# Performance work log

Hardware: AMD Instinct MI355X
Metric: run time of the kernel (lower is better)

Reference implementation:

```python
import jax, jax.numpy as jnp
import numpy as np

H = 16      # num_heads
HD = 128    # head_dim = embed_dim // num_heads
BS = 64     # NSA block_size
SEL = 8     # selected blocks per query (block_counts)
WIN = 64    # sliding window (left) size
BASE = 10000.0


def _rope(t):
    # t: [b, n, h, hd]; rotary LRPE (lrpe_type=1)
    n, hd = t.shape[1], t.shape[-1]
    half = hd // 2
    inv = 1.0 / (BASE ** (jnp.arange(half, dtype=jnp.float32) / half))
    th = jnp.arange(n, dtype=jnp.float32)[:, None] * inv[None, :]  # [n, half]
    cos = jnp.cos(th)[None, :, None, :]
    sin = jnp.sin(th)[None, :, None, :]
    t1, t2 = t[..., :half], t[..., half:]
    return jnp.concatenate([t1 * cos - t2 * sin, t1 * sin + t2 * cos], axis=-1)


def _nsa_forward(x, Wq, Wk, Wv, Wg, Wo):
    b, n, d = x.shape
    nb = n // BS
    scale = HD ** -0.5
    q = (x @ Wq).reshape(b, n, H, HD)
    k = (x @ Wk).reshape(b, n, H, HD)
    v = (x @ Wv).reshape(b, n, H, HD)
    g = jax.nn.sigmoid(x @ Wg)                   # [b, n, 3H]
    g_cmp, g_slc, g_swa = jnp.split(g, 3, axis=-1)
    q = _rope(q)
    k = _rope(k)
    idx = jnp.arange(n)

    # --- compression branch: mean-pooled KV blocks, causal over fully-past blocks
    k_cmp = k.reshape(b, nb, BS, H, HD).mean(axis=2)   # [b, nb, h, hd]
    v_cmp = v.reshape(b, nb, BS, H, HD).mean(axis=2)
    s_cmp = jnp.einsum('bnhd,bmhd->bhnm', q, k_cmp) * scale  # [b, h, n, nb]
    blk_end = (jnp.arange(nb) + 1) * BS - 1
    cmp_mask = idx[:, None] >= blk_end[None, :]        # [n, nb]
    p_cmp = jax.nn.softmax(jnp.where(cmp_mask[None, None], s_cmp, -1e30), axis=-1)
    p_cmp = p_cmp * cmp_mask.any(-1)[None, None, :, None]  # zero rows with no valid block
    o_cmp = jnp.einsum('bhnm,bmhd->bnhd', p_cmp, v_cmp)

    # --- selection branch: top-k blocks by compressed scores, current block forced
    cur_blk = jax.nn.one_hot(idx // BS, nb, dtype=jnp.float32)  # [n, nb]
    imp = p_cmp + 2.0 * cur_blk[None, None]
    sel = jax.lax.top_k(imp, SEL)[1]                   # [b, h, n, SEL]
    blk_sel = jax.nn.one_hot(sel, nb).sum(-2) > 0      # [b, h, n, nb]
    causal = idx[:, None] >= idx[None, :]              # [n, n]
    slc_mask = blk_sel[..., idx // BS] & causal[None, None]  # [b, h, n, n]
    s_full = jnp.einsum('bnhd,bmhd->bhnm', q, k) * scale     # [b, h, n, n]
    p_slc = jax.nn.softmax(jnp.where(slc_mask, s_full, -1e30), axis=-1)
    o_slc = jnp.einsum('bhnm,bmhd->bnhd', p_slc, v)

    swa_mask = causal & (idx[:, None] - idx[None, :] <= WIN)
    p_swa = jax.nn.softmax(jnp.where(swa_mask[None, None], s_full, -1e30), axis=-1)
    o_swa = jnp.einsum('bhnm,bmhd->bnhd', p_swa, v)

    o = (o_cmp * g_cmp[..., None] + o_slc * g_slc[..., None]
         + o_swa * g_swa[..., None])                   # [b, n, h, hd]
    return o.reshape(b, n, H * HD) @ Wo


def setup_inputs() -> dict:
    key = jax.random.key(0)
    ks = jax.random.split(key, 6)
    B, N, D = 2, 1024, 2048
    std = 0.02
    return {
        'x': jax.random.normal(ks[0], (B, N, D), jnp.float32),
        'Wq': jax.random.normal(ks[1], (D, H * HD), jnp.float32) * std,
        'Wk': jax.random.normal(ks[2], (D, H * HD), jnp.float32) * std,
        'Wv': jax.random.normal(ks[3], (D, H * HD), jnp.float32) * std,
        'Wg': jax.random.normal(ks[4], (D, 3 * H), jnp.float32) * std,
        'Wo': jax.random.normal(ks[5], (H * HD, D), jnp.float32) * std,
    }


def reference(x, Wq, Wk, Wv, Wg, Wo):
    return _nsa_forward(x, Wq, Wk, Wv, Wg, Wo)
```

## Files before the change

### kernel.cpp

```cpp
#include <hip/hip_runtime.h>
#include <hip/hip_bf16.h>

#define HN   16
#define HDIM 128
#define NSEQ 1024
#define NBLK 16
#define BSZ  64
#define SCALE 0.08838834764831845f
#define QKV_STR 6400
#define KOFS 2048
#define VOFS 4096
#define GOFS 6144

typedef __attribute__((ext_vector_type(8))) short bfrag;
typedef __attribute__((ext_vector_type(4))) float facc;

__device__ __forceinline__ float bf2f(short s) {
  union { unsigned u; float f; } cv;
  cv.u = ((unsigned)(unsigned short)s) << 16;
  return cv.f;
}
__device__ __forceinline__ short f2bf(float f) {
  unsigned u = __float_as_uint(f);
  u = (u + 0x7fff + ((u >> 16) & 1)) >> 16;
  return (short)u;
}

#define ASYNC16(gp, lp)                                                    \
  __builtin_amdgcn_global_load_lds(                                        \
      (const __attribute__((address_space(1))) void*)(gp),                 \
      (__attribute__((address_space(3))) void*)(lp), 16, 0, 0)

#define MFMA16(a, b, c) __builtin_amdgcn_mfma_f32_16x16x32_bf16(a, b, c, 0, 0, 0)

__global__ __launch_bounds__(256) void prep(const float* __restrict__ Wq,
                                            const float* __restrict__ Wk,
                                            const float* __restrict__ Wv,
                                            const float* __restrict__ Wg,
                                            const float* __restrict__ Wo,
                                            const float* __restrict__ x,
                                            short* __restrict__ w_t,
                                            short* __restrict__ wo_t,
                                            short* __restrict__ x_bf,
                                            float2* __restrict__ tbl) {
  __shared__ float tile[32][33];
  const int z = blockIdx.z;
  const int bx = blockIdx.x * 32, by = blockIdx.y * 32;
  const int tx = threadIdx.x & 31, ty = threadIdx.x >> 5;
  if (z == 5) {
    if (blockIdx.y >= 4) return;
    int i = (blockIdx.y * 64 + blockIdx.x) * 256 + threadIdx.x;
    int d = i & 63, n = i >> 6;
    float inv = expf(-(float)d * (9.210340371976184f / 64.0f));
    float sn, cs;
    sincosf((float)n * inv, &sn, &cs);
    tbl[i] = make_float2(cs, sn);
    return;
  }
  if (z == 4) {
#pragma unroll
    for (int i = 0; i < 4; ++i) {
      const int row = by + ty + 8 * i;
      x_bf[(size_t)row * 2048 + bx + tx] = f2bf(x[(size_t)row * 2048 + bx + tx]);
    }
    return;
  }
  if (z == 3) {
    if (blockIdx.x >= 4) return;
#pragma unroll
    for (int i = 0; i < 4; ++i) {
      const int c = bx + tx;
      tile[ty + 8 * i][tx] = (c < 48) ? Wg[(size_t)(by + ty + 8 * i) * 48 + c] : 0.f;
    }
    __syncthreads();
#pragma unroll
    for (int i = 0; i < 4; ++i)
      w_t[(size_t)(GOFS + bx + ty + 8 * i) * 2048 + by + tx] = f2bf(tile[tx][ty + 8 * i]);
    return;
  }
  if (z == 6) {
#pragma unroll
    for (int i = 0; i < 4; ++i)
      tile[ty + 8 * i][tx] = Wo[(size_t)(by + ty + 8 * i) * 2048 + bx + tx];
    __syncthreads();
#pragma unroll
    for (int i = 0; i < 4; ++i)
      wo_t[(size_t)(bx + ty + 8 * i) * 2048 + by + tx] = f2bf(tile[tx][ty + 8 * i]);
    return;
  }
  const float* src = (z == 0) ? Wq : (z == 1) ? Wk : Wv;
#pragma unroll
  for (int i = 0; i < 4; ++i)
    tile[ty + 8 * i][tx] = src[(size_t)(by + ty + 8 * i) * 2048 + bx + tx];
  __syncthreads();
#pragma unroll
  for (int i = 0; i < 4; ++i)
    w_t[(size_t)(z * 2048 + bx + ty + 8 * i) * 2048 + by + tx] = f2bf(tile[tx][ty + 8 * i]);
}

__global__ __launch_bounds__(512, 1) void gemm256(const short* __restrict__ A,
                                                  const short* __restrict__ Bt,
                                                  short* __restrict__ C,
                                                  int M, int N, int K) {
  __shared__ short lds[2][2][16384];
  const int t = threadIdx.x;
  const int l = t & 63, w = t >> 6;
  const int wm = w >> 2, wn = w & 3;
  const int lm = l & 15, hi = l >> 4;
  const int lanexor = (lm & 7) << 3;
  const int kk0 = (hi * 8) ^ lanexor;
  const int L = blockIdx.x;
  const int item = (L & 7) * (gridDim.x >> 3) + (L >> 3);
  const int nrow = M >> 8;
  const int row0 = (item % nrow) * 256, col0 = (item / nrow) * 256;
  const int nt = K >> 6;
  const int ni = nt >> 1;

  const int srow = t >> 3;
  const int scol = 8 * ((t & 7) ^ (srow & 7));
  const short* Ab = A + (size_t)(row0 + srow) * K + scol;
  const short* Bb = Bt + (size_t)(col0 + srow) * K + scol;

#define STAGE(mat, srcbase, h, tau, buf)                                     \
  {                                                                          \
    const short* g_ = (srcbase) + (size_t)(h) * 128 * K + (size_t)(tau) * 64;\
    short* d_ = &lds[buf][mat][(h) * 8192 + t * 8];                          \
    ASYNC16(g_, d_);                                                         \
    ASYNC16(g_ + (size_t)64 * K, d_ + 4096);                                 \
  }

#define DS_A(qm, cb)                                                         \
  _Pragma("unroll") for (int ii = 0; ii < 4; ++ii) {                         \
    const int row_ = wm * 128 + (qm) * 64 + ii * 16 + lm;                    \
    af[ii * 2 + 0] = *(const bfrag*)&lds[cb][0][row_ * 64 + kk0];            \
    af[ii * 2 + 1] = *(const bfrag*)&lds[cb][0][row_ * 64 + (kk0 ^ 32)];     \
  }
#define DS_B(qn, arr, cb)                                                    \
  _Pragma("unroll") for (int jj = 0; jj < 2; ++jj) {                         \
    const int row_ = wn * 64 + (qn) * 32 + jj * 16 + lm;                     \
    arr[jj * 2 + 0] = *(const bfrag*)&lds[cb][1][row_ * 64 + kk0];           \
    arr[jj * 2 + 1] = *(const bfrag*)&lds[cb][1][row_ * 64 + (kk0 ^ 32)];    \
  }
#define QUAD(qm, qn, arr)                                                    \
  _Pragma("unroll") for (int ii = 0; ii < 4; ++ii)                           \
  _Pragma("unroll") for (int jj = 0; jj < 2; ++jj) {                         \
    acc[(qm)*4+ii][(qn)*2+jj] = MFMA16(af[ii*2+0], arr[jj*2+0], acc[(qm)*4+ii][(qn)*2+jj]); \
    acc[(qm)*4+ii][(qn)*2+jj] = MFMA16(af[ii*2+1], arr[jj*2+1], acc[(qm)*4+ii][(qn)*2+jj]); \
  }
#define BARLG                                                                \
  __builtin_amdgcn_s_barrier();                                              \
  asm volatile("s_waitcnt lgkmcnt(0)" ::: "memory");                         \
  __builtin_amdgcn_sched_barrier(0)
#define PRIO1 __builtin_amdgcn_s_setprio(1)
#define PRIO0 __builtin_amdgcn_s_setprio(0)
#define BAR __builtin_amdgcn_s_barrier()

  facc acc[8][4] = {};
  bfrag af[8], bf0[4], bf1[4];

  STAGE(0, Ab, 0, 0, 0); STAGE(0, Ab, 1, 0, 0);
  STAGE(1, Bb, 0, 0, 0); STAGE(1, Bb, 1, 0, 0);
  STAGE(1, Bb, 0, 1, 1); STAGE(1, Bb, 1, 1, 1);
  asm volatile("s_waitcnt vmcnt(4)" ::: "memory");
  BAR;

  for (int i = 0; i < ni; ++i) {
    const int t1 = 2 * i + 1;
    const int g2 = (2 * i + 2 < nt) ? 2 * i + 2 : 2 * i;
    const int g3 = (2 * i + 3 < nt) ? 2 * i + 3 : t1;

    DS_A(0, 0); DS_B(0, bf0, 0);
    STAGE(0, Ab, 0, t1, 1);
    BARLG; PRIO1; QUAD(0, 0, bf0); PRIO0; BAR;

    DS_B(1, bf1, 0);
    STAGE(0, Ab, 1, t1, 1);
    BARLG; PRIO1; QUAD(0, 1, bf1); PRIO0; BAR;

    DS_A(1, 0);
    STAGE(1, Bb, 0, g2, 0);
    BARLG; PRIO1; QUAD(1, 1, bf1); PRIO0; BAR;

    STAGE(1, Bb, 1, g2, 0);
    PRIO1; QUAD(1, 0, bf0); PRIO0;
    asm volatile("s_waitcnt vmcnt(4)" ::: "memory");
    BAR;

    DS_A(0, 1); DS_B(0, bf0, 1);
    STAGE(0, Ab, 0, g2, 0);
    BARLG; PRIO1; QUAD(0, 0, bf0); PRIO0; BAR;

    DS_B(1, bf1, 1);
    STAGE(0, Ab, 1, g2, 0);
    BARLG; PRIO1; QUAD(0, 1, bf1); PRIO0; BAR;

    DS_A(1, 1);
    STAGE(1, Bb, 0, g3, 1);
    BARLG; PRIO1; QUAD(1, 1, bf1); PRIO0; BAR;

    STAGE(1, Bb, 1, g3, 1);
    PRIO1; QUAD(1, 0, bf0); PRIO0;
    asm volatile("s_waitcnt vmcnt(4)" ::: "memory");
    BAR;
  }

#pragma unroll
  for (int i = 0; i < 8; ++i)
#pragma unroll
    for (int j = 0; j < 4; ++j)
#pragma unroll
      for (int rr = 0; rr < 4; ++rr)
        C[(size_t)(row0 + wm * 128 + i * 16 + hi * 4 + rr) * N +
          col0 + wn * 64 + j * 16 + lm] = f2bf(acc[i][j][rr]);
#undef STAGE
#undef DS_A
#undef DS_B
#undef QUAD
#undef BARLG
#undef PRIO1
#undef PRIO0
#undef BAR
}

__device__ __forceinline__ void store_c(float* p, float v) { *p = v; }
__device__ __forceinline__ void store_c(short* p, float v) { *p = f2bf(v); }

template <typename OT>
__global__ __launch_bounds__(512, 1) void gemm_bf16_bt(const short* __restrict__ A,
                                                       const short* __restrict__ Bt,
                                                       OT* __restrict__ C,
                                                       int M, int N, int K) {
  __shared__ short As[128 * 32];
  __shared__ short Bs[128 * 32];
  const int t = threadIdx.x;
  const int l = t & 63, w = t >> 6;
  const int wr = w >> 2, wc = w & 3;
  const int lm = l & 15, lk = (l >> 4) * 8;
  const int nwg = gridDim.x;
  const int L = blockIdx.x;
  const int wg = (L & 7) * (nwg >> 3) + (L >> 3);
  const int nrow = M >> 7;
  const int row0 = (wg % nrow) * 128, col0 = (wg / nrow) * 128;
  facc acc[4][2] = {};

  const int sr = t >> 2;
  const int sk = (t & 3) * 8;
  const short* Ag = A + (size_t)(row0 + sr) * K + sk;
  const short* Bg = Bt + (size_t)(col0 + sr) * K + sk;
  short* la = As + t * 8;
  short* lb = Bs + t * 8;

  for (int k0 = 0; k0 < K; k0 += 32) {
    ASYNC16(Ag + k0, la);
    ASYNC16(Bg + k0, lb);
    __syncthreads();
    bfrag af[4], bf[2];
#pragma unroll
    for (int i = 0; i < 4; ++i)
      af[i] = *(const bfrag*)&As[(wr * 64 + i * 16 + lm) * 32 + lk];
#pragma unroll
    for (int j = 0; j < 2; ++j)
      bf[j] = *(const bfrag*)&Bs[(wc * 32 + j * 16 + lm) * 32 + lk];
#pragma unroll
    for (int i = 0; i < 4; ++i)
#pragma unroll
      for (int j = 0; j < 2; ++j)
        acc[i][j] = MFMA16(af[i], bf[j], acc[i][j]);
    __syncthreads();
  }

  const int orow = row0 + wr * 64 + (l >> 4) * 4;
  const int ocol = col0 + wc * 32 + lm;
#pragma unroll
  for (int i = 0; i < 4; ++i)
#pragma unroll
    for (int j = 0; j < 2; ++j)
#pragma unroll
      for (int rr = 0; rr < 4; ++rr)
        store_c(&C[(size_t)(orow + i * 16 + rr) * N + ocol + j * 16], acc[i][j][rr]);
}

__global__ __launch_bounds__(256) void postqkv(short* __restrict__ qkv,
                                               const float2* __restrict__ tbl,
                                               float* __restrict__ kc,
                                               short* __restrict__ vt,
                                               short* __restrict__ vct) {
  const int nb = blockIdx.x, h = blockIdx.y, b = blockIdx.z;
  const int t = threadIdx.x;
  const int n0 = nb * 64;
  __shared__ short tile[64][136];

  const int row = t >> 2;
  const int c16 = (t & 3) * 16;
  const float2* tp = tbl + (size_t)(n0 + row) * 64 + c16;

#pragma unroll
  for (int qk = 0; qk < 2; ++qk) {
    short* base = qkv + (size_t)(b * NSEQ + n0 + row) * QKV_STR + qk * KOFS + h * HDIM + c16;
    bfrag lo0 = *(const bfrag*)base;
    bfrag lo1 = *(const bfrag*)(base + 8);
    bfrag hi0 = *(const bfrag*)(base + 64);
    bfrag hi1 = *(const bfrag*)(base + 72);
    bfrag olo0, olo1, ohi0, ohi1;
#pragma unroll
    for (int j = 0; j < 8; ++j) {
      float2 cs0 = tp[j], cs1 = tp[j + 8];
      float a0 = bf2f(lo0[j]), b0 = bf2f(hi0[j]);
      float a1 = bf2f(lo1[j]), b1 = bf2f(hi1[j]);
      olo0[j] = f2bf(a0 * cs0.x - b0 * cs0.y);
      ohi0[j] = f2bf(a0 * cs0.y + b0 * cs0.x);
      olo1[j] = f2bf(a1 * cs1.x - b1 * cs1.y);
      ohi1[j] = f2bf(a1 * cs1.y + b1 * cs1.x);
    }
    *(bfrag*)base = olo0;
    *(bfrag*)(base + 8) = olo1;
    *(bfrag*)(base + 64) = ohi0;
    *(bfrag*)(base + 72) = ohi1;
    if (qk == 1) {
      *(bfrag*)&tile[row][c16] = olo0;
      *(bfrag*)&tile[row][c16 + 8] = olo1;
      *(bfrag*)&tile[row][c16 + 64] = ohi0;
      *(bfrag*)&tile[row][c16 + 72] = ohi1;
    }
  }
  __syncthreads();

  if (t < 128) {
    float s = 0.f;
#pragma unroll 8
    for (int r = 0; r < 64; ++r) s += bf2f(tile[r][t]);
    kc[(((size_t)(b * NBLK + nb) * HN) + h) * 128 + t] = s * (1.0f / 64.0f);
  }
  __syncthreads();

#pragma unroll
  for (int it = 0; it < 4; ++it) {
    int idx = t + 256 * it;
    int r2 = idx >> 4, ch = idx & 15;
    *(bfrag*)&tile[r2][ch * 8] =
        *(const bfrag*)&qkv[(size_t)(b * NSEQ + n0 + r2) * QKV_STR + VOFS + h * HDIM + ch * 8];
  }
  __syncthreads();

#pragma unroll
  for (int it = 0; it < 4; ++it) {
    int idx = t + 256 * it;
    int d = idx >> 3, ch = idx & 7;
    bfrag tv;
    float s = 0.f;
#pragma unroll
    for (int j = 0; j < 8; ++j) {
      tv[j] = tile[ch * 8 + j][d];
      s += bf2f(tv[j]);
    }
    *(bfrag*)&vt[(((size_t)(b * HN + h) * 128) + d) * 1024 + n0 + ch * 8] = tv;
    s += __shfl_down(s, 4);
    s += __shfl_down(s, 2);
    s += __shfl_down(s, 1);
    if ((t & 7) == 0)
      vct[(((size_t)(b * HN + h) * 128) + d) * 16 + nb] = f2bf(s * (1.0f / 64.0f));
  }
}

__global__ __launch_bounds__(64) void cmp_sel(const short* __restrict__ qkv,
                                              const float* __restrict__ kc,
                                              short* __restrict__ pc,
                                              int* __restrict__ sel) {
  int i = blockIdx.x * 64 + threadIdx.x;
  int n = i & 1023;
  int h = (i >> 10) & 15;
  int b = i >> 14;
  const short* qp = qkv + (size_t)(b * NSEQ + n) * QKV_STR + h * HDIM;
  const int nv = (n + 1) >> 6;
  float s[NBLK];
#pragma unroll
  for (int m = 0; m < NBLK; ++m) s[m] = 0.f;
  for (int d0 = 0; d0 < HDIM; d0 += 8) {
    bfrag qv = *(const bfrag*)&qp[d0];
    float qf[8];
#pragma unroll
    for (int dd = 0; dd < 8; ++dd) qf[dd] = bf2f(qv[dd]);
    for (int m = 0; m < nv; ++m) {
      const float4* kp = (const float4*)(kc + ((size_t)((b * NBLK + m) * HN + h) << 7) + d0);
      const float4 k0 = kp[0], k1 = kp[1];
      s[m] += qf[0] * k0.x + qf[1] * k0.y + qf[2] * k0.z + qf[3] * k0.w +
              qf[4] * k1.x + qf[5] * k1.y + qf[6] * k1.z + qf[7] * k1.w;
    }
  }
  float mx = -1e30f;
  for (int m = 0; m < nv; ++m) { s[m] *= SCALE; mx = fmaxf(mx, s[m]); }
  float den = 0.f;
  for (int m = 0; m < nv; ++m) { s[m] = __expf(s[m] - mx); den += s[m]; }
  const float rden = (nv > 0) ? 1.0f / den : 0.f;
  float p[NBLK];
#pragma unroll
  for (int m = 0; m < NBLK; ++m) p[m] = (m < nv) ? s[m] * rden : 0.f;
  bfrag o0, o1;
#pragma unroll
  for (int m = 0; m < 8; ++m) { o0[m] = f2bf(p[m]); o1[m] = f2bf(p[m + 8]); }
  bfrag* pout = (bfrag*)(pc + (size_t)i * 16);
  pout[0] = o0; pout[1] = o1;
  p[n >> 6] += 2.0f;
  int mask = 0;
#pragma unroll
  for (int ss = 0; ss < 8; ++ss) {
    int best = 0;
    float bv = -1e30f;
#pragma unroll
    for (int m = 0; m < NBLK; ++m)
      if (p[m] > bv) { bv = p[m]; best = m; }
    mask |= 1 << best;
    p[best] = -1e30f;
  }
  sel[i] = mask;
}

__global__ __launch_bounds__(512, 1) void attn_mfma(
    const short* __restrict__ qkv, const short* __restrict__ vt,
    const short* __restrict__ vct, const short* __restrict__ pc,
    const int* __restrict__ sel, short* __restrict__ o) {
  const int fid = blockIdx.x;
  const int xcd = fid & 7;
  const int idx = fid >> 3;
  const int pair = (xcd << 2) | (idx & 3);
  const int rblk = idx >> 2;
  const int h = pair & 15, b = pair >> 4;

  const int tid = threadIdx.x;
  const int wid = tid >> 6;
  const int l = tid & 63;
  const int lm = l & 15, hi = l >> 4;
  const int rt = wid * 8 + rblk;
  const int nbase = rt * 16;
  const int CTMAX = ((56 + rblk) * 16) >> 6;

  __shared__ short kbuf[2][8192];
  __shared__ short vbuf[2][8192];
  __shared__ short pbuf[8][2][1024];
  short* p_slc = &pbuf[wid][0][0];
  short* p_swa = &pbuf[wid][1][0];

  const short* qrow = qkv + (size_t)(b * NSEQ + nbase + lm) * QKV_STR + h * HDIM;
  bfrag qf[4];
#pragma unroll
  for (int ks = 0; ks < 4; ++ks) qf[ks] = *(const bfrag*)&qrow[32 * ks + 8 * hi];

  int selrow = sel[(size_t)(b * HN + h) * NSEQ + nbase + lm];
  int uni = selrow;
#pragma unroll
  for (int m = 1; m < 16; m <<= 1) uni |= __shfl_xor(uni, m);
  int sel4[4];
#pragma unroll
  for (int rg = 0; rg < 4; ++rg) sel4[rg] = __shfl(selrow, 4 * hi + rg);

  const int thi = nbase >> 6;
  const int tlo = (nbase >= 64) ? ((nbase - 64) >> 6) : 0;
  const int wmask = (int)((2u << thi) - (1u << tlo));
  const unsigned am = (unsigned)(uni | wmask) & (unsigned)((2u << thi) - 1);

  facc acc_slc[8] = {}, acc_swa[8] = {};
  float ps_s[4] = {0.f, 0.f, 0.f, 0.f}, ps_w[4] = {0.f, 0.f, 0.f, 0.f};

#define STAGEKV(ct_, buf_)                                                   \
  {                                                                          \
    _Pragma("unroll") for (int rr = 0; rr < 2; ++rr) {                       \
      const int i2 = tid + 512 * rr;                                         \
      const int rw = i2 >> 4, cc = i2 & 15;                                  \
      const short* g_ = qkv + (size_t)(b * NSEQ + (ct_) * 64 + rw) * QKV_STR \
                        + KOFS + h * HDIM + 8 * (cc ^ (rw & 7));             \
      ASYNC16(g_, &kbuf[buf_][i2 * 8]);                                      \
    }                                                                        \
    _Pragma("unroll") for (int rr = 0; rr < 2; ++rr) {                       \
      const int i2 = tid + 512 * rr;                                         \
      const int dd = i2 >> 3, cc = i2 & 7;                                   \
      const short* g_ = vt + ((size_t)(b * HN + h) * 128 + dd) * 1024        \
                        + (ct_) * 64 + 8 * (cc ^ (dd & 7));                  \
      ASYNC16(g_, &vbuf[buf_][i2 * 8]);                                      \
    }                                                                        \
  }

#define EXPF(f_)                                                            \
  _Pragma("unroll") for (int rg = 0; rg < 4; ++rg) {                        \
    const int col_ = ct * 64 + 16 * (f_) + lm;                              \
    const int row_ = nbase + 4 * hi + rg;                                   \
    float e_ = __expf(sacc[f_][rg] * SCALE);                                \
    e_ = (col_ <= row_) ? e_ : 0.f;                                         \
    float es_ = ((sel4[rg] >> ct) & 1) ? e_ : 0.f;                          \
    float ew_ = (row_ - col_ <= 64) ? e_ : 0.f;                             \
    ps_s[rg] += es_;                                                        \
    ps_w[rg] += ew_;                                                        \
    const int srow_ = 4 * hi + rg;                                          \
    const int sidx_ = (64 * srow_ + 16 * (f_) + lm) ^ ((srow_ & 7) << 3);   \
    if (do_s) p_slc[sidx_] = f2bf(es_);                                     \
    if (do_w) p_swa[sidx_] = f2bf(ew_);                                     \
  }

  STAGEKV(0, 0);
  asm volatile("s_waitcnt vmcnt(0)" ::: "memory");
  __syncthreads();

  for (int ct = 0; ct <= CTMAX; ++ct) {
    const int cur = ct & 1;
    if (ct < CTMAX) STAGEKV(ct + 1, cur ^ 1);

    if ((am >> ct) & 1) {
      const bool do_s = (uni >> ct) & 1;
      const bool do_w = (wmask >> ct) & 1;

      facc sacc[4] = {};
#pragma unroll
      for (int f = 0; f < 4; ++f) {
        const int row_ = 16 * f + lm;
        const int rx = row_ & 7;
        bfrag k0 = *(const bfrag*)&kbuf[cur][row_ * 128 + 8 * ((0 + hi) ^ rx)];
        bfrag k1 = *(const bfrag*)&kbuf[cur][row_ * 128 + 8 * ((4 + hi) ^ rx)];
        bfrag k2 = *(const bfrag*)&kbuf[cur][row_ * 128 + 8 * ((8 + hi) ^ rx)];
        bfrag k3 = *(const bfrag*)&kbuf[cur][row_ * 128 + 8 * ((12 + hi) ^ rx)];
        sacc[f] = MFMA16(qf[0], k0, sacc[f]);
        sacc[f] = MFMA16(qf[1], k1, sacc[f]);
        sacc[f] = MFMA16(qf[2], k2, sacc[f]);
        sacc[f] = MFMA16(qf[3], k3, sacc[f]);
      }

      EXPF(0); EXPF(1); EXPF(2); EXPF(3);

#pragma unroll
      for (int ks = 0; ks < 2; ++ks) {
        const int ridx = (64 * lm + 8 * hi + 32 * ks) ^ ((lm & 7) << 3);
        bfrag pas = {}, paw = {};
        if (do_s) pas = *(const bfrag*)&p_slc[ridx];
        if (do_w) paw = *(const bfrag*)&p_swa[ridx];
#pragma unroll
        for (int df = 0; df < 8; ++df) {
          const int d_ = 16 * df + lm;
          bfrag vb = *(const bfrag*)&vbuf[cur][d_ * 64 + 8 * ((4 * ks + hi) ^ (d_ & 7))];
          if (do_s) acc_slc[df] = MFMA16(pas, vb, acc_slc[df]);
          if (do_w) acc_swa[df] = MFMA16(paw, vb, acc_swa[df]);
        }
      }
    }

    asm volatile("s_waitcnt vmcnt(0)" ::: "memory");
    __syncthreads();
  }
#undef STAGEKV
#undef EXPF

  facc acc_cmp[8] = {};
  {
    bfrag pa = {};
    if (hi < 2)
      pa = *(const bfrag*)&pc[((size_t)(b * HN + h) * NSEQ + nbase + lm) * 16 + 8 * hi];
#pragma unroll
    for (int df = 0; df < 8; ++df) {
      bfrag vb = {};
      if (hi < 2)
        vb = *(const bfrag*)&vct[(((size_t)(b * HN + h) * 128) + 16 * df + lm) * 16 + 8 * hi];
      acc_cmp[df] = MFMA16(pa, vb, acc_cmp[df]);
    }
  }

#pragma unroll
  for (int m = 1; m < 16; m <<= 1) {
#pragma unroll
    for (int rg = 0; rg < 4; ++rg) {
      ps_s[rg] += __shfl_xor(ps_s[rg], m);
      ps_w[rg] += __shfl_xor(ps_w[rg], m);
    }
  }

  float inv_s[4], inv_w[4], gcv[4], gsv[4], gwv[4];
#pragma unroll
  for (int rg = 0; rg < 4; ++rg) {
    inv_s[rg] = 1.0f / ps_s[rg];
    inv_w[rg] = 1.0f / ps_w[rg];
    const short* gp = qkv + (size_t)(b * NSEQ + nbase + 4 * hi + rg) * QKV_STR + GOFS;
    gcv[rg] = 1.0f / (1.0f + __expf(-bf2f(gp[h])));
    gsv[rg] = 1.0f / (1.0f + __expf(-bf2f(gp[16 + h])));
    gwv[rg] = 1.0f / (1.0f + __expf(-bf2f(gp[32 + h])));
  }

  short* obase = o + (size_t)(b * NSEQ + nbase) * 2048 + h * HDIM;
#pragma unroll
  for (int df = 0; df < 8; ++df)
#pragma unroll
    for (int rg = 0; rg < 4; ++rg) {
      float val = gcv[rg] * acc_cmp[df][rg] +
                  gsv[rg] * acc_slc[df][rg] * inv_s[rg] +
                  gwv[rg] * acc_swa[df][rg] * inv_w[rg];
      obase[(size_t)(4 * hi + rg) * 2048 + 16 * df + lm] = f2bf(val);
    }
}

extern "C" void kernel_launch(void* const* d_in, const int* in_sizes, int n_in,
                              void* d_out, int out_size, void* d_ws, size_t ws_size,
                              hipStream_t stream) {
  const float* x  = (const float*)d_in[0];
  const float* Wq = (const float*)d_in[1];
  const float* Wk = (const float*)d_in[2];
  const float* Wv = (const float*)d_in[3];
  const float* Wg = (const float*)d_in[4];
  const float* Wo = (const float*)d_in[5];
  float* out = (float*)d_out;

  char* w = (char*)d_ws;
  short* x_bf = (short*)w;
  short* o_bf = x_bf;
  w += (size_t)2048 * 2048 * 2;
  short* w_t  = (short*)w;
  w += (size_t)6400 * 2048 * 2;
  short* qkv  = (short*)w;
  w += (size_t)2048 * 6400 * 2;
  float* kc   = (float*)w; w += (size_t)65536 * 4;
  short* vct  = (short*)w; w += (size_t)65536 * 2;
  short* pcb  = (short*)w; w += (size_t)524288 * 2;
  int*   sel  = (int*)w;   w += (size_t)32768 * 4;
  short* vt   = (short*)w; w += (size_t)4194304 * 2;
  float2* tbl = (float2*)w; w += (size_t)65536 * 8;
  short* wo_t = (short*)w; w += (size_t)2048 * 2048 * 2;

  const dim3 blk(256);
  prep<<<dim3(64, 64, 7), blk, 0, stream>>>(Wq, Wk, Wv, Wg, Wo, x, w_t, wo_t, x_bf, tbl);
  gemm256<<<200, dim3(512), 0, stream>>>(x_bf, w_t, qkv, 2048, 6400, 2048);
  postqkv<<<dim3(16, 16, 2), blk, 0, stream>>>(qkv, tbl, kc, vt, vct);
  cmp_sel<<<512, dim3(64), 0, stream>>>(qkv, kc, pcb, sel);
  attn_mfma<<<256, dim3(512), 0, stream>>>(qkv, vt, vct, pcb, sel, o_bf);
  gemm_bf16_bt<float><<<256, dim3(512), 0, stream>>>(o_bf, wo_t, out, 2048, 2048, 2048);
}
```

Measured before the change: 227.4 us.

## Triple-buffer KV staging in attention kernel and remap GEMM tile-to-XCD assignment

The attention kernel's K/V shared-memory staging goes from double to triple buffering. Each tile is prefetched two iterations ahead and the code waits only on the older batch of loads (vmcnt(4)), so global-memory latency overlaps more compute. Separately, the GEMM workgroup-to-tile mapping is changed to a fixed XCD-aware layout that groups row/column tiles per XCD for L2 reuse. The extra buffer raises LDS use, and the hardcoded GEMM tile mapping assumes a specific grid shape (a 16x16 tile grid).

```diff
diff --git a/kernel.cpp b/kernel.cpp
--- a/kernel.cpp
+++ b/kernel.cpp
@@ -236,11 +236,11 @@
   const int l = t & 63, w = t >> 6;
   const int wr = w >> 2, wc = w & 3;
   const int lm = l & 15, lk = (l >> 4) * 8;
-  const int nwg = gridDim.x;
   const int L = blockIdx.x;
-  const int wg = (L & 7) * (nwg >> 3) + (L >> 3);
-  const int nrow = M >> 7;
-  const int row0 = (wg % nrow) * 128, col0 = (wg / nrow) * 128;
+  const int xcd = L & 7, j = L >> 3;
+  const int rowt = (xcd & 3) * 4 + (j & 3);
+  const int colt = (xcd >> 2) * 8 + (j >> 2);
+  const int row0 = rowt * 128, col0 = colt * 128;
   facc acc[4][2] = {};
 
   const int sr = t >> 2;
@@ -259,13 +259,13 @@
     for (int i = 0; i < 4; ++i)
       af[i] = *(const bfrag*)&As[(wr * 64 + i * 16 + lm) * 32 + lk];
 #pragma unroll
-    for (int j = 0; j < 2; ++j)
-      bf[j] = *(const bfrag*)&Bs[(wc * 32 + j * 16 + lm) * 32 + lk];
+    for (int j2 = 0; j2 < 2; ++j2)
+      bf[j2] = *(const bfrag*)&Bs[(wc * 32 + j2 * 16 + lm) * 32 + lk];
 #pragma unroll
     for (int i = 0; i < 4; ++i)
 #pragma unroll
-      for (int j = 0; j < 2; ++j)
-        acc[i][j] = MFMA16(af[i], bf[j], acc[i][j]);
+      for (int j2 = 0; j2 < 2; ++j2)
+        acc[i][j2] = MFMA16(af[i], bf[j2], acc[i][j2]);
     __syncthreads();
   }
 
@@ -274,10 +274,10 @@
 #pragma unroll
   for (int i = 0; i < 4; ++i)
 #pragma unroll
-    for (int j = 0; j < 2; ++j)
+    for (int j2 = 0; j2 < 2; ++j2)
 #pragma unroll
       for (int rr = 0; rr < 4; ++rr)
-        store_c(&C[(size_t)(orow + i * 16 + rr) * N + ocol + j * 16], acc[i][j][rr]);
+        store_c(&C[(size_t)(orow + i * 16 + rr) * N + ocol + j2 * 16], acc[i][j2][rr]);
 }
 
 __global__ __launch_bounds__(256) void postqkv(short* __restrict__ qkv,
@@ -434,8 +434,8 @@
   const int nbase = rt * 16;
   const int CTMAX = ((56 + rblk) * 16) >> 6;
 
-  __shared__ short kbuf[2][8192];
-  __shared__ short vbuf[2][8192];
+  __shared__ short kbuf[3][8192];
+  __shared__ short vbuf[3][8192];
   __shared__ short pbuf[8][2][1024];
   short* p_slc = &pbuf[wid][0][0];
   short* p_swa = &pbuf[wid][1][0];
@@ -496,12 +496,18 @@
   }
 
   STAGEKV(0, 0);
-  asm volatile("s_waitcnt vmcnt(0)" ::: "memory");
+  STAGEKV(1, 1);
+  asm volatile("s_waitcnt vmcnt(4)" ::: "memory");
   __syncthreads();
 
+  int cur = 0;
   for (int ct = 0; ct <= CTMAX; ++ct) {
-    const int cur = ct & 1;
-    if (ct < CTMAX) STAGEKV(ct + 1, cur ^ 1);
+    const bool have_next2 = (ct + 2 <= CTMAX);
+    if (have_next2) {
+      const int nb2 = (cur + 2 >= 3) ? cur - 1 : cur + 2;
+      const int ct2 = ct + 2;
+      STAGEKV(ct2, nb2);
+    }
 
     if ((am >> ct) & 1) {
       const bool do_s = (uni >> ct) & 1;
@@ -540,8 +546,14 @@
       }
     }
 
-    asm volatile("s_waitcnt vmcnt(0)" ::: "memory");
-    __syncthreads();
+    if (ct < CTMAX) {
+      if (have_next2)
+        asm volatile("s_waitcnt vmcnt(4)" ::: "memory");
+      else
+        asm volatile("s_waitcnt vmcnt(0)" ::: "memory");
+      __syncthreads();
+    }
+    cur = (cur + 1 >= 3) ? 0 : cur + 1;
   }
 #undef STAGEKV
 #undef EXPF
```

Result: no change. 226.5 us (median of 2 runs) (-0.4%).
